# Optimization experiments

Hardware: AMD Instinct MI355X
Metric: run time of the kernel (lower is better)

The kernel has to match this reference:

```python
import jax, jax.numpy as jnp
import numpy as np

B, L, H, R = 8, 8256, 768, 24  # L = 128*129/2 flattened token-pair positions


def setup_inputs() -> dict:
    key = jax.random.key(0)
    k1, k2, k3 = jax.random.split(key, 3)
    hidden_state = jax.random.normal(k1, (B, L, H), dtype=jnp.float32)
    # per-relation Linear(hidden_size, 3) weights, stacked: (R, 3, H), (R, 3)
    W = jax.random.normal(k2, (R, 3, H), dtype=jnp.float32) * 0.02
    b = jax.random.normal(k3, (R, 3), dtype=jnp.float32) * 0.02
    return {"hidden_state": hidden_state, "W": W, "b": b}


def reference(hidden_state, W, b):
    # Batched equivalent of the per-relation Linear loop + stack(dim=1):
    # logits[b, r, l, t] = sum_h hidden_state[b,l,h] * W[r,t,h] + b[r,t]
    logits = jnp.einsum('blh,rth->brlt', hidden_state, W) + b[None, :, None, :]
    return jax.nn.softmax(logits, axis=-1)  # (B, R, L, 3)
```

## Files before the change

### kernel.cpp

```cpp
#include <hip/hip_runtime.h>
#include <hip/hip_bf16.h>


#define HD     768
#define LSEQ   8256
#define RREL   24
#define KSTEPS 24
#define NT     5
#define NCOL   72
#define HALFK  12
#define CHUNKS 3840

typedef float f32x4 __attribute__((ext_vector_type(4)));
typedef short s16x8 __attribute__((ext_vector_type(8)));
typedef int   i32x4 __attribute__((ext_vector_type(4)));

__device__ __forceinline__ unsigned f2bf_rne(float f) {
  unsigned u = __builtin_bit_cast(unsigned, f);
  u += 0x7FFFu + ((u >> 16) & 1u);
  return u >> 16;
}

__device__ __forceinline__ int pack2(float lo, float hi) {
  unsigned l = __bfloat16_as_ushort(__float2bfloat16(lo));
  unsigned h = __bfloat16_as_ushort(__float2bfloat16(hi));
  return (int)(l | (h << 16));
}

__global__ void conv_w_kernel(const float* __restrict__ W,
                              unsigned short* __restrict__ wsB) {
  int idx = blockIdx.x * 256 + threadIdx.x;
  if (idx >= KSTEPS * NT * 64) return;
  int ks   = idx / (NT * 64);
  int rem  = idx - ks * (NT * 64);
  int nt   = rem >> 6;
  int lane = rem & 63;
  int col  = nt * 16 + (lane & 15);
  int k0   = ks * 32 + (lane >> 4) * 8;
  unsigned short v[8] = {0, 0, 0, 0, 0, 0, 0, 0};
  if (col < NCOL) {
    const float* p = W + (size_t)col * HD + k0;
    float4 a = *(const float4*)p;
    float4 b = *(const float4*)(p + 4);
    v[0] = (unsigned short)f2bf_rne(a.x); v[1] = (unsigned short)f2bf_rne(a.y);
    v[2] = (unsigned short)f2bf_rne(a.z); v[3] = (unsigned short)f2bf_rne(a.w);
    v[4] = (unsigned short)f2bf_rne(b.x); v[5] = (unsigned short)f2bf_rne(b.y);
    v[6] = (unsigned short)f2bf_rne(b.z); v[7] = (unsigned short)f2bf_rne(b.w);
  }
  *(s16x8*)(wsB + (size_t)idx * 8) = *(s16x8*)v;
}

#define ALOAD(ks) do { if ((ks) < KSTEPS) {                        \
    const int s_ = (ks) % 5, o_ = (ks) * 32;                       \
    abuf[s_][0][0] = *(const float4*)(pA0 + o_);                   \
    abuf[s_][0][1] = *(const float4*)(pA0 + o_ + 4);               \
    abuf[s_][1][0] = *(const float4*)(pA1 + o_);                   \
    abuf[s_][1][1] = *(const float4*)(pA1 + o_ + 4);               \
  } } while (0)

#define COMPUTE(ks, kl) do {                                        \
    s16x8 af_[2];                                                   \
    _Pragma("unroll")                                               \
    for (int mt_ = 0; mt_ < 2; ++mt_) {                             \
      float4 a0 = abuf[(ks) % 5][mt_][0], a1 = abuf[(ks) % 5][mt_][1]; \
      i32x4 av;                                                     \
      av[0] = __builtin_amdgcn_ds_bpermute(bp, pack2(a0.x, a0.y));  \
      av[1] = __builtin_amdgcn_ds_bpermute(bp, pack2(a0.z, a0.w));  \
      av[2] = __builtin_amdgcn_ds_bpermute(bp, pack2(a1.x, a1.y));  \
      av[3] = __builtin_amdgcn_ds_bpermute(bp, pack2(a1.z, a1.w));  \
      af_[mt_] = __builtin_bit_cast(s16x8, av);                     \
    }                                                               \
    _Pragma("unroll")                                               \
    for (int nt_ = 0; nt_ < NT; ++nt_) {                            \
      s16x8 bf_ = __builtin_bit_cast(s16x8,                         \
          shB[((kl) * NT + nt_) * 64 + lane]);                      \
      acc[0][nt_] = __builtin_amdgcn_mfma_f32_16x16x32_bf16(af_[0], bf_, acc[0][nt_], 0, 0, 0); \
      acc[1][nt_] = __builtin_amdgcn_mfma_f32_16x16x32_bf16(af_[1], bf_, acc[1][nt_], 0, 0, 0); \
    }                                                               \
  } while (0)

__global__ __launch_bounds__(256, 2)
void tagging_ws(const float* __restrict__ hs, const float* __restrict__ bias,
                const i32x4* __restrict__ pWS, float* __restrict__ out) {
  __shared__ i32x4 shB[CHUNKS];

  const int tid  = threadIdx.x;
  const int lane = tid & 63;
  const int wid  = tid >> 6;
  const int m0   = blockIdx.x * 128 + wid * 32;

  const float* pA0 = hs + (size_t)(m0 + (lane >> 2)) * HD + (lane & 3) * 8;
  const float* pA1 = pA0 + 16 * HD;
  const int bp = ((lane & 15) * 4 + (lane >> 4)) * 4;

  f32x4  acc[2][NT] = {};
  float4 abuf[5][2][2];

  #pragma unroll
  for (int i = 0; i < 15; ++i) shB[tid + i * 256] = pWS[tid + i * 256];
  ALOAD(0); ALOAD(1); ALOAD(2); ALOAD(3);
  __syncthreads();

  #pragma unroll
  for (int ks = 0; ks < HALFK; ++ks) { ALOAD(ks + 4); COMPUTE(ks, ks); }

  __syncthreads();
  #pragma unroll
  for (int i = 0; i < 15; ++i) shB[tid + i * 256] = pWS[CHUNKS + tid + i * 256];
  __syncthreads();

  #pragma unroll
  for (int ks = HALFK; ks < KSTEPS; ++ks) { ALOAD(ks + 4); COMPUTE(ks, ks - HALFK); }

  __syncthreads();

  float* lgf = (float*)shB;
  #pragma unroll
  for (int mt = 0; mt < 2; ++mt)
    #pragma unroll
    for (int nt = 0; nt < NT; ++nt)
      #pragma unroll
      for (int j = 0; j < 4; ++j)
        lgf[(wid * 32 + mt * 16 + (lane >> 4) * 4 + j) * 85 + nt * 16 + (lane & 15)]
            = acc[mt][nt][j];

  const int bidx = m0 / LSEQ;
  const int l0   = m0 - bidx * LSEQ;
  #pragma unroll
  for (int it = 0; it < 12; ++it) {
    int flat = it * 64 + lane;
    int g    = flat >> 5;
    int tokl = flat & 31;
    const float* row = lgf + (wid * 32 + tokl) * 85;
    float x0 = row[3 * g + 0] + bias[3 * g + 0];
    float x1 = row[3 * g + 1] + bias[3 * g + 1];
    float x2 = row[3 * g + 2] + bias[3 * g + 2];
    float mx = fmaxf(x0, fmaxf(x1, x2));
    float e0 = __expf(x0 - mx), e1 = __expf(x1 - mx), e2 = __expf(x2 - mx);
    float inv = 1.0f / (e0 + e1 + e2);
    size_t o = ((size_t)(bidx * RREL + g) * LSEQ + l0 + tokl) * 3;
    out[o + 0] = e0 * inv;
    out[o + 1] = e1 * inv;
    out[o + 2] = e2 * inv;
  }
}

__global__ __launch_bounds__(64, 2)
void tagging_fb(const float* __restrict__ hs, const float* __restrict__ W,
                const float* __restrict__ bias, float* __restrict__ out) {
  __shared__ float lg[32][85];
  const int lane = threadIdx.x;
  const int m0   = blockIdx.x * 32;

  const float* pA0 = hs + (size_t)(m0 + (lane >> 2)) * HD + (lane & 3) * 8;
  const float* pA1 = pA0 + 16 * HD;
  const int bp = ((lane & 15) * 4 + (lane >> 4)) * 4;

  const float* pB[NT];
  #pragma unroll
  for (int nt = 0; nt < NT; ++nt)
    pB[nt] = W + (size_t)(nt * 16 + (lane & 15)) * HD + (lane >> 4) * 8;
  const bool b4ok = (lane & 15) < 8;

  f32x4  acc[2][NT] = {};
  float4 abuf[5][2][2];
  float4 fbf[2][NT][2];

#define FB_BLOAD(ks) do { if ((ks) < KSTEPS) {                     \
    _Pragma("unroll")                                              \
    for (int nt_ = 0; nt_ < 4; ++nt_) {                            \
      fbf[(ks) & 1][nt_][0] = *(const float4*)(pB[nt_] + (ks)*32); \
      fbf[(ks) & 1][nt_][1] = *(const float4*)(pB[nt_] + (ks)*32 + 4); \
    }                                                              \
    if (b4ok) {                                                    \
      fbf[(ks) & 1][4][0] = *(const float4*)(pB[4] + (ks)*32);     \
      fbf[(ks) & 1][4][1] = *(const float4*)(pB[4] + (ks)*32 + 4); \
    } else {                                                       \
      fbf[(ks) & 1][4][0] = make_float4(0.f,0.f,0.f,0.f);          \
      fbf[(ks) & 1][4][1] = make_float4(0.f,0.f,0.f,0.f);          \
    }                                                              \
  } } while (0)

  ALOAD(0); ALOAD(1); ALOAD(2); ALOAD(3);
  FB_BLOAD(0);

  #pragma unroll
  for (int ks = 0; ks < KSTEPS; ++ks) {
    ALOAD(ks + 4);
    FB_BLOAD(ks + 1);
    s16x8 af[2];
    #pragma unroll
    for (int mt = 0; mt < 2; ++mt) {
      float4 a0 = abuf[ks % 5][mt][0], a1 = abuf[ks % 5][mt][1];
      i32x4 av;
      av[0] = __builtin_amdgcn_ds_bpermute(bp, pack2(a0.x, a0.y));
      av[1] = __builtin_amdgcn_ds_bpermute(bp, pack2(a0.z, a0.w));
      av[2] = __builtin_amdgcn_ds_bpermute(bp, pack2(a1.x, a1.y));
      av[3] = __builtin_amdgcn_ds_bpermute(bp, pack2(a1.z, a1.w));
      af[mt] = __builtin_bit_cast(s16x8, av);
    }
    #pragma unroll
    for (int nt = 0; nt < NT; ++nt) {
      float4 b0 = fbf[ks & 1][nt][0], b1 = fbf[ks & 1][nt][1];
      i32x4 bv;
      bv[0] = pack2(b0.x, b0.y); bv[1] = pack2(b0.z, b0.w);
      bv[2] = pack2(b1.x, b1.y); bv[3] = pack2(b1.z, b1.w);
      s16x8 bf = __builtin_bit_cast(s16x8, bv);
      acc[0][nt] = __builtin_amdgcn_mfma_f32_16x16x32_bf16(af[0], bf, acc[0][nt], 0, 0, 0);
      acc[1][nt] = __builtin_amdgcn_mfma_f32_16x16x32_bf16(af[1], bf, acc[1][nt], 0, 0, 0);
    }
  }

  #pragma unroll
  for (int mt = 0; mt < 2; ++mt)
    #pragma unroll
    for (int nt = 0; nt < NT; ++nt)
      #pragma unroll
      for (int j = 0; j < 4; ++j)
        lg[mt * 16 + (lane >> 4) * 4 + j][nt * 16 + (lane & 15)] = acc[mt][nt][j];
  __syncthreads();

  const int bidx = m0 / LSEQ;
  const int l0   = m0 - bidx * LSEQ;
  #pragma unroll
  for (int it = 0; it < 12; ++it) {
    int flat = it * 64 + lane;
    int g    = flat >> 5;
    int tokl = flat & 31;
    float x0 = lg[tokl][3 * g + 0] + bias[3 * g + 0];
    float x1 = lg[tokl][3 * g + 1] + bias[3 * g + 1];
    float x2 = lg[tokl][3 * g + 2] + bias[3 * g + 2];
    float mx = fmaxf(x0, fmaxf(x1, x2));
    float e0 = __expf(x0 - mx), e1 = __expf(x1 - mx), e2 = __expf(x2 - mx);
    float inv = 1.0f / (e0 + e1 + e2);
    size_t o = ((size_t)(bidx * RREL + g) * LSEQ + l0 + tokl) * 3;
    out[o + 0] = e0 * inv;
    out[o + 1] = e1 * inv;
    out[o + 2] = e2 * inv;
  }
}

extern "C" void kernel_launch(void* const* d_in, const int* in_sizes, int n_in,
                              void* d_out, int out_size, void* d_ws, size_t ws_size,
                              hipStream_t stream) {
  (void)in_sizes; (void)n_in; (void)out_size;
  const float* hs   = (const float*)d_in[0];
  const float* W    = (const float*)d_in[1];
  const float* bias = (const float*)d_in[2];
  float* out = (float*)d_out;

  const size_t needB = (size_t)KSTEPS * NT * 64 * 8 * 2;
  if (d_ws && ws_size >= needB) {
    hipLaunchKernelGGL(conv_w_kernel, dim3(30), dim3(256), 0, stream,
                       W, (unsigned short*)d_ws);
    hipLaunchKernelGGL(tagging_ws, dim3(516), dim3(256), 0, stream,
                       hs, bias, (const i32x4*)d_ws, out);
  } else {
    hipLaunchKernelGGL(tagging_fb, dim3(2064), dim3(64), 0, stream,
                       hs, W, bias, out);
  }
}
```

Baseline: 54.42 us.

## Split K across two waves per 32-row tile and stream B from global

Replaces the 4-wave, 128-row block that staged all bf16 weights in LDS with a 2-wave, 32-row block where each wave handles half of the K dimension and reads its B fragments directly from the global workspace, double-buffered in registers. The partial accumulators are combined through shared memory before the softmax epilogue. This removes the large LDS weight staging and its barriers, cuts LDS use to raise occupancy, and quadruples the grid. In exchange it adds a cross-wave reduction and repeated global/L2 reads of the weights per block. The A prefetch depth also drops from 4 to 2 steps.

```diff
diff --git a/kernel.cpp b/kernel.cpp
--- a/kernel.cpp
+++ b/kernel.cpp
@@ -6,10 +6,9 @@
 #define LSEQ   8256
 #define RREL   24
 #define KSTEPS 24
+#define WKS    12
 #define NT     5
 #define NCOL   72
-#define HALFK  12
-#define CHUNKS 3840
 
 typedef float f32x4 __attribute__((ext_vector_type(4)));
 typedef short s16x8 __attribute__((ext_vector_type(8)));
@@ -50,88 +49,108 @@
   *(s16x8*)(wsB + (size_t)idx * 8) = *(s16x8*)v;
 }
 
-#define ALOAD(ks) do { if ((ks) < KSTEPS) {                        \
-    const int s_ = (ks) % 5, o_ = (ks) * 32;                       \
+#define ALOAD(ks, LIM) do { if ((ks) < (LIM)) {                    \
+    const int s_ = (ks) % 3, o_ = (ks) * 32;                       \
     abuf[s_][0][0] = *(const float4*)(pA0 + o_);                   \
     abuf[s_][0][1] = *(const float4*)(pA0 + o_ + 4);               \
     abuf[s_][1][0] = *(const float4*)(pA1 + o_);                   \
     abuf[s_][1][1] = *(const float4*)(pA1 + o_ + 4);               \
   } } while (0)
 
-#define COMPUTE(ks, kl) do {                                        \
-    s16x8 af_[2];                                                   \
-    _Pragma("unroll")                                               \
-    for (int mt_ = 0; mt_ < 2; ++mt_) {                             \
-      float4 a0 = abuf[(ks) % 5][mt_][0], a1 = abuf[(ks) % 5][mt_][1]; \
-      i32x4 av;                                                     \
-      av[0] = __builtin_amdgcn_ds_bpermute(bp, pack2(a0.x, a0.y));  \
-      av[1] = __builtin_amdgcn_ds_bpermute(bp, pack2(a0.z, a0.w));  \
-      av[2] = __builtin_amdgcn_ds_bpermute(bp, pack2(a1.x, a1.y));  \
-      av[3] = __builtin_amdgcn_ds_bpermute(bp, pack2(a1.z, a1.w));  \
-      af_[mt_] = __builtin_bit_cast(s16x8, av);                     \
-    }                                                               \
-    _Pragma("unroll")                                               \
-    for (int nt_ = 0; nt_ < NT; ++nt_) {                            \
-      s16x8 bf_ = __builtin_bit_cast(s16x8,                         \
-          shB[((kl) * NT + nt_) * 64 + lane]);                      \
-      acc[0][nt_] = __builtin_amdgcn_mfma_f32_16x16x32_bf16(af_[0], bf_, acc[0][nt_], 0, 0, 0); \
-      acc[1][nt_] = __builtin_amdgcn_mfma_f32_16x16x32_bf16(af_[1], bf_, acc[1][nt_], 0, 0, 0); \
-    }                                                               \
+#define BLOAD_WS(ks, LIM) do { if ((ks) < (LIM)) {                 \
+    _Pragma("unroll")                                              \
+    for (int nt_ = 0; nt_ < NT; ++nt_)                             \
+      bbuf[(ks) & 1][nt_] = pW4[(ks) * NT * 64 + nt_ * 64 + lane]; \
+  } } while (0)
+
+#define AFRAG(ks, af)  do {                                        \
+    _Pragma("unroll")                                              \
+    for (int mt_ = 0; mt_ < 2; ++mt_) {                            \
+      float4 a0 = abuf[(ks) % 3][mt_][0], a1 = abuf[(ks) % 3][mt_][1]; \
+      i32x4 av;                                                    \
+      av[0] = __builtin_amdgcn_ds_bpermute(bp, pack2(a0.x, a0.y)); \
+      av[1] = __builtin_amdgcn_ds_bpermute(bp, pack2(a0.z, a0.w)); \
+      av[2] = __builtin_amdgcn_ds_bpermute(bp, pack2(a1.x, a1.y)); \
+      av[3] = __builtin_amdgcn_ds_bpermute(bp, pack2(a1.z, a1.w)); \
+      (af)[mt_] = __builtin_bit_cast(s16x8, av);                   \
+    }                                                              \
   } while (0)
 
-__global__ __launch_bounds__(256, 2)
-void tagging_ws(const float* __restrict__ hs, const float* __restrict__ bias,
+__global__ __launch_bounds__(128, 4)
+void tagging_ks(const float* __restrict__ hs, const float* __restrict__ bias,
                 const i32x4* __restrict__ pWS, float* __restrict__ out) {
-  __shared__ i32x4 shB[CHUNKS];
+  __shared__ float sh[32 * 85];
 
   const int tid  = threadIdx.x;
   const int lane = tid & 63;
   const int wid  = tid >> 6;
-  const int m0   = blockIdx.x * 128 + wid * 32;
-
-  const float* pA0 = hs + (size_t)(m0 + (lane >> 2)) * HD + (lane & 3) * 8;
+  const int m0   = blockIdx.x * 32;
+
+  const float* pA0 = hs + (size_t)(m0 + (lane >> 2)) * HD
+                        + wid * (WKS * 32) + (lane & 3) * 8;
   const float* pA1 = pA0 + 16 * HD;
+  const i32x4* pW4 = pWS + (size_t)wid * WKS * NT * 64;
   const int bp = ((lane & 15) * 4 + (lane >> 4)) * 4;
 
   f32x4  acc[2][NT] = {};
-  float4 abuf[5][2][2];
-
-  #pragma unroll
-  for (int i = 0; i < 15; ++i) shB[tid + i * 256] = pWS[tid + i * 256];
-  ALOAD(0); ALOAD(1); ALOAD(2); ALOAD(3);
+  float4 abuf[3][2][2];
+  i32x4  bbuf[2][NT];
+
+  ALOAD(0, WKS); ALOAD(1, WKS);
+  BLOAD_WS(0, WKS);
+
+  #pragma unroll
+  for (int ks = 0; ks < WKS; ++ks) {
+    ALOAD(ks + 2, WKS);
+    BLOAD_WS(ks + 1, WKS);
+    s16x8 af[2];
+    AFRAG(ks, af);
+    #pragma unroll
+    for (int nt = 0; nt < NT; ++nt) {
+      s16x8 bf = __builtin_bit_cast(s16x8, bbuf[ks & 1][nt]);
+      acc[0][nt] = __builtin_amdgcn_mfma_f32_16x16x32_bf16(af[0], bf, acc[0][nt], 0, 0, 0);
+      acc[1][nt] = __builtin_amdgcn_mfma_f32_16x16x32_bf16(af[1], bf, acc[1][nt], 0, 0, 0);
+    }
+  }
+
+  if (wid == 0) {
+    #pragma unroll
+    for (int mt = 0; mt < 2; ++mt)
+      #pragma unroll
+      for (int nt = 0; nt < NT; ++nt)
+        #pragma unroll
+        for (int j = 0; j < 4; ++j)
+          sh[((mt * NT + nt) * 4 + j) * 64 + lane] = acc[mt][nt][j];
+  }
   __syncthreads();
 
-  #pragma unroll
-  for (int ks = 0; ks < HALFK; ++ks) { ALOAD(ks + 4); COMPUTE(ks, ks); }
-
+  if (wid == 1) {
+    #pragma unroll
+    for (int mt = 0; mt < 2; ++mt)
+      #pragma unroll
+      for (int nt = 0; nt < NT; ++nt)
+        #pragma unroll
+        for (int j = 0; j < 4; ++j)
+          acc[mt][nt][j] += sh[((mt * NT + nt) * 4 + j) * 64 + lane];
+    #pragma unroll
+    for (int mt = 0; mt < 2; ++mt)
+      #pragma unroll
+      for (int nt = 0; nt < NT; ++nt)
+        #pragma unroll
+        for (int j = 0; j < 4; ++j)
+          sh[(mt * 16 + (lane >> 4) * 4 + j) * 85 + nt * 16 + (lane & 15)]
+              = acc[mt][nt][j];
+  }
   __syncthreads();
-  #pragma unroll
-  for (int i = 0; i < 15; ++i) shB[tid + i * 256] = pWS[CHUNKS + tid + i * 256];
-  __syncthreads();
-
-  #pragma unroll
-  for (int ks = HALFK; ks < KSTEPS; ++ks) { ALOAD(ks + 4); COMPUTE(ks, ks - HALFK); }
-
-  __syncthreads();
-
-  float* lgf = (float*)shB;
-  #pragma unroll
-  for (int mt = 0; mt < 2; ++mt)
-    #pragma unroll
-    for (int nt = 0; nt < NT; ++nt)
-      #pragma unroll
-      for (int j = 0; j < 4; ++j)
-        lgf[(wid * 32 + mt * 16 + (lane >> 4) * 4 + j) * 85 + nt * 16 + (lane & 15)]
-            = acc[mt][nt][j];
 
   const int bidx = m0 / LSEQ;
   const int l0   = m0 - bidx * LSEQ;
   #pragma unroll
-  for (int it = 0; it < 12; ++it) {
-    int flat = it * 64 + lane;
+  for (int it = 0; it < 6; ++it) {
+    int flat = it * 128 + tid;
     int g    = flat >> 5;
     int tokl = flat & 31;
-    const float* row = lgf + (wid * 32 + tokl) * 85;
+    const float* row = sh + tokl * 85;
     float x0 = row[3 * g + 0] + bias[3 * g + 0];
     float x1 = row[3 * g + 1] + bias[3 * g + 1];
     float x2 = row[3 * g + 2] + bias[3 * g + 2];
@@ -163,7 +182,7 @@
   const bool b4ok = (lane & 15) < 8;
 
   f32x4  acc[2][NT] = {};
-  float4 abuf[5][2][2];
+  float4 abuf[3][2][2];
   float4 fbf[2][NT][2];
 
 #define FB_BLOAD(ks) do { if ((ks) < KSTEPS) {                     \
@@ -181,24 +200,15 @@
     }                                                              \
   } } while (0)
 
-  ALOAD(0); ALOAD(1); ALOAD(2); ALOAD(3);
+  ALOAD(0, KSTEPS); ALOAD(1, KSTEPS);
   FB_BLOAD(0);
 
   #pragma unroll
   for (int ks = 0; ks < KSTEPS; ++ks) {
-    ALOAD(ks + 4);
+    ALOAD(ks + 2, KSTEPS);
     FB_BLOAD(ks + 1);
     s16x8 af[2];
-    #pragma unroll
-    for (int mt = 0; mt < 2; ++mt) {
-      float4 a0 = abuf[ks % 5][mt][0], a1 = abuf[ks % 5][mt][1];
-      i32x4 av;
-      av[0] = __builtin_amdgcn_ds_bpermute(bp, pack2(a0.x, a0.y));
-      av[1] = __builtin_amdgcn_ds_bpermute(bp, pack2(a0.z, a0.w));
-      av[2] = __builtin_amdgcn_ds_bpermute(bp, pack2(a1.x, a1.y));
-      av[3] = __builtin_amdgcn_ds_bpermute(bp, pack2(a1.z, a1.w));
-      af[mt] = __builtin_bit_cast(s16x8, av);
-    }
+    AFRAG(ks, af);
     #pragma unroll
     for (int nt = 0; nt < NT; ++nt) {
       float4 b0 = fbf[ks & 1][nt][0], b1 = fbf[ks & 1][nt][1];
@@ -253,7 +263,7 @@
   if (d_ws && ws_size >= needB) {
     hipLaunchKernelGGL(conv_w_kernel, dim3(30), dim3(256), 0, stream,
                        W, (unsigned short*)d_ws);
-    hipLaunchKernelGGL(tagging_ws, dim3(516), dim3(256), 0, stream,
+    hipLaunchKernelGGL(tagging_ks, dim3(2064), dim3(128), 0, stream,
                        hs, bias, (const i32x4*)d_ws, out);
   } else {
     hipLaunchKernelGGL(tagging_fb, dim3(2064), dim3(64), 0, stream,
```

Result: slower. 56.03 us (+2.9%).
